# Performance work log

Measured on AMD Instinct MI355X. Metric: run time of the kernel, lower is better.

The kernel has to match this reference:

```python
import jax, jax.numpy as jnp
import numpy as np

N, D, K = 10000, 784, 16          # nodes, input feat dim, num_neighbors
E = N * (K - 1)                   # edges
H = 128                           # hidden width in all MLPs
SIZES = [784, 128, 2]             # node_sizes


def setup_inputs() -> dict:
    key = jax.random.key(0)
    ks = jax.random.split(key, 24)
    w = lambda k, shape: jax.random.normal(k, shape, jnp.float32) * 0.02
    inp = {
        "x": jax.random.normal(ks[0], (N, D), jnp.float32),
        "edge_attr": jax.random.uniform(ks[1], (E, 1), jnp.float32),
        "idxs": jax.random.randint(ks[2], (N, K - 1), 0, N, dtype=jnp.int32),
    }
    # Layer 1: in=784, msg_size=784, out=128
    inp["l1_msg_w1"] = w(ks[3], (D + 1, H));      inp["l1_msg_b1"] = jnp.zeros((H,), jnp.float32)
    inp["l1_msg_w2"] = w(ks[4], (H, D));          inp["l1_msg_b2"] = jnp.zeros((D,), jnp.float32)
    inp["l1_node_w1"] = w(ks[5], (D + D, H));     inp["l1_node_b1"] = jnp.zeros((H,), jnp.float32)
    inp["l1_node_w2"] = w(ks[6], (H, 128));       inp["l1_node_b2"] = jnp.zeros((128,), jnp.float32)
    # Layer 2: in=128, msg_size=128, out=2
    inp["l2_msg_w1"] = w(ks[7], (128 + 1, H));    inp["l2_msg_b1"] = jnp.zeros((H,), jnp.float32)
    inp["l2_msg_w2"] = w(ks[8], (H, 128));        inp["l2_msg_b2"] = jnp.zeros((128,), jnp.float32)
    inp["l2_node_w1"] = w(ks[9], (128 + 128, H)); inp["l2_node_b1"] = jnp.zeros((H,), jnp.float32)
    inp["l2_node_w2"] = w(ks[10], (H, 2));        inp["l2_node_b2"] = jnp.zeros((2,), jnp.float32)
    return inp


def _mlp(x, w1, b1, w2, b2):
    return jax.nn.relu(x @ w1 + b1) @ w2 + b2


def _node_layer(x, src, edge_attr,
                mw1, mb1, mw2, mb2, nw1, nb1, nw2, nb2):
    # message over edges: cat(x[src], edge_attr) -> MLP   [E, msg_size]
    msg = _mlp(jnp.concatenate([x[src], edge_attr], axis=1), mw1, mb1, mw2, mb2)
    # scatter_mean by src index (faithful to the original, which uses index=src)
    sums = jax.ops.segment_sum(msg, src, num_segments=N)
    cnt = jax.ops.segment_sum(jnp.ones((src.shape[0], 1), msg.dtype), src, num_segments=N)
    agg = jnp.where(cnt > 0, sums / jnp.maximum(cnt, 1.0), 0.0)
    # node update: cat(x, agg_msg) -> MLP
    return _mlp(jnp.concatenate([x, agg], axis=1), nw1, nb1, nw2, nb2)


def reference(x, edge_attr, idxs,
              l1_msg_w1, l1_msg_b1, l1_msg_w2, l1_msg_b2,
              l1_node_w1, l1_node_b1, l1_node_w2, l1_node_b2,
              l2_msg_w1, l2_msg_b1, l2_msg_w2, l2_msg_b2,
              l2_node_w1, l2_node_b1, l2_node_w2, l2_node_b2):
    src = idxs.reshape(-1)  # [E]; dst is unused by the original message computation
    h = _node_layer(x, src, edge_attr,
                    l1_msg_w1, l1_msg_b1, l1_msg_w2, l1_msg_b2,
                    l1_node_w1, l1_node_b1, l1_node_w2, l1_node_b2)
    proj = _node_layer(h, src, edge_attr,
                       l2_msg_w1, l2_msg_b1, l2_msg_w2, l2_msg_b2,
                       l2_node_w1, l2_node_b1, l2_node_w2, l2_node_b2)  # [N, 2]
    # vectorized per-neighbor squared distances (replaces the nested python loop)
    neigh = proj[idxs]                                   # [N, K-1, 2]
    d = jnp.sum((proj[:, None, :] - neigh) ** 2, axis=-1)  # [N, K-1]
    return d.reshape(-1, 1)                              # [N*(K-1), 1]
```

## Files before the change

kernel.cpp:

```cpp
#include <hip/hip_runtime.h>

#define N_NODES 10000
#define E_EDGES 150000
#define KNB     15
#define EBLOCKS 587
#define GEMM_BLOCKS 628

__global__ void count_kernel(const int* __restrict__ idxs, int* __restrict__ cnt, int e) {
    int i = blockIdx.x * blockDim.x + threadIdx.x;
    if (i < e) atomicAdd(&cnt[idxs[i]], 1);
}

__device__ __forceinline__
void gemm_tile2(const float* __restrict__ A, int K,
                const float* __restrict__ Blo, const float* __restrict__ Bhi, int ldB,
                float* __restrict__ C, int ldC, int M,
                int rowBlk, int colBlk) {
    __shared__ float As2[16][34];
    __shared__ float Bs2[16][64];
    int tid = threadIdx.x;
    int tn  = tid & 15, tm = tid >> 4;
    int arow = tid >> 3, acB = (tid & 7) << 1;
    int brow = tid >> 4, bcol = (tid & 15) << 2;
    int rowBase = rowBlk * 32, colBase = colBlk * 64;

    bool half = (Bhi != nullptr) && (colBase >= 128);
    const float* B = half ? Bhi : Blo;
    int bj = colBase - (half ? 128 : 0) + bcol;

    float2 av; float4 bv;
    auto loadA = [&](int k0, float2& dst) {
        int gr = rowBase + arow;
        if (gr < M) dst = *(const float2*)(A + (size_t)gr * K + k0 + acB);
        else { dst.x = dst.y = 0.f; }
    };
    auto loadB = [&](int k0, float4& dst) {
        dst = *(const float4*)(B + (size_t)(k0 + brow) * ldB + bj);
    };
    loadA(0, av); loadB(0, bv);

    float acc[2][4] = {};
    for (int k0 = 0; k0 < K; k0 += 16) {
        __syncthreads();
        As2[acB + 0][arow] = av.x; As2[acB + 1][arow] = av.y;
        *(float4*)&Bs2[brow][bcol] = bv;
        __syncthreads();
        if (k0 + 16 < K) { loadA(k0 + 16, av); loadB(k0 + 16, bv); }
#pragma unroll
        for (int k = 0; k < 16; ++k) {
            float4 b = *(const float4*)&Bs2[k][tn << 2];
            float2 a = *(const float2*)&As2[k][tm << 1];
            acc[0][0] = fmaf(a.x, b.x, acc[0][0]); acc[0][1] = fmaf(a.x, b.y, acc[0][1]);
            acc[0][2] = fmaf(a.x, b.z, acc[0][2]); acc[0][3] = fmaf(a.x, b.w, acc[0][3]);
            acc[1][0] = fmaf(a.y, b.x, acc[1][0]); acc[1][1] = fmaf(a.y, b.y, acc[1][1]);
            acc[1][2] = fmaf(a.y, b.z, acc[1][2]); acc[1][3] = fmaf(a.y, b.w, acc[1][3]);
        }
    }
#pragma unroll
    for (int i = 0; i < 2; ++i) {
        int row = rowBase + tm * 2 + i;
        if (row >= M) continue;
#pragma unroll
        for (int j = 0; j < 4; ++j)
            C[(size_t)row * ldC + colBase + (tn << 2) + j] = acc[i][j];
    }
}

__global__ __launch_bounds__(256)
void scanfold_kernel(const float* __restrict__ mw2, const float* __restrict__ mb2,
                     const float* __restrict__ nw1, const float* __restrict__ nb2,
                     const float* __restrict__ nw2,
                     const float* __restrict__ m2w1, const float* __restrict__ m2b1,
                     const float* __restrict__ m2w2, const float* __restrict__ m2b2,
                     const float* __restrict__ n2w1, const float* __restrict__ n2b1,
                     float* __restrict__ M1, float* __restrict__ M2,
                     float* __restrict__ WH,
                     float* __restrict__ v1, float* __restrict__ v2,
                     float* __restrict__ bu2, float* __restrict__ bx2,
                     const int* __restrict__ cnt, int* __restrict__ eoff,
                     float* __restrict__ maskv, int* __restrict__ fillc) {
    int b = blockIdx.x;
    if (b == 0) {
        __shared__ int ssum[256];
        int tid = threadIdx.x;
        const int CH = 40;
        int base = tid * CH;
        int v[CH]; int s = 0;
#pragma unroll
        for (int q = 0; q < CH; ++q) {
            int i = base + q;
            v[q] = (i < N_NODES) ? cnt[i] : 0;
            s += v[q];
        }
        ssum[tid] = s;
        __syncthreads();
        for (int off = 1; off < 256; off <<= 1) {
            int t = (tid >= off) ? ssum[tid - off] : 0;
            __syncthreads();
            ssum[tid] += t;
            __syncthreads();
        }
        int ex = ssum[tid] - s;
#pragma unroll
        for (int q = 0; q < CH; ++q) {
            int i = base + q;
            if (i < N_NODES) {
                eoff[i]  = ex;
                maskv[i] = (v[q] > 0) ? 1.f : 0.f;
                fillc[i] = 0;
                ex += v[q];
            }
        }
        return;
    }
    b -= 1;
    if (b < 8) {
        gemm_tile2(mw2, 784, nw1 + 784 * 128, nullptr, 128, M1, 128, 128, b >> 1, b & 1);
    } else if (b < 16) {
        int t = b - 8;
        gemm_tile2(m2w2, 128, n2w1 + 128 * 128, nullptr, 128, M2, 128, 128, t >> 1, t & 1);
    } else if (b < 32) {
        int t = b - 16;
        gemm_tile2(nw2, 128, m2w1, n2w1, 128, WH, 256, 128, t >> 2, t & 3);
    } else {
        __shared__ float red[256];
        int t  = (b - 32) >> 1;
        int j  = ((b - 32) & 1) * 64 + (threadIdx.x & 63);
        int kq = threadIdx.x >> 6;
        const float* bvec; const float* Bv; const float* add; float* out; int Kv;
        if (t == 0)      { bvec = mb2;  Bv = nw1 + 784 * 128;  add = nullptr; out = v1;  Kv = 784; }
        else if (t == 1) { bvec = m2b2; Bv = n2w1 + 128 * 128; add = nullptr; out = v2;  Kv = 128; }
        else if (t == 2) { bvec = nb2;  Bv = m2w1;             add = m2b1;    out = bu2; Kv = 128; }
        else             { bvec = nb2;  Bv = n2w1;             add = n2b1;    out = bx2; Kv = 128; }
        float acc = 0.f;
        for (int k = kq; k < Kv; k += 4) acc = fmaf(bvec[k], Bv[k * 128 + j], acc);
        red[threadIdx.x] = acc;
        __syncthreads();
        if (threadIdx.x < 64) {
            float tot = red[threadIdx.x] + red[threadIdx.x + 64] +
                        red[threadIdx.x + 128] + red[threadIdx.x + 192];
            out[j] = tot + (add ? add[j] : 0.f);
        }
    }
}

__device__ __forceinline__
void gemm784_tile(const float* __restrict__ A,
                  const float* __restrict__ B0, const float* __restrict__ B1,
                  const float* __restrict__ biasLo, const float* __restrict__ biasHi,
                  const float* __restrict__ vhi, const float* __restrict__ rowmask,
                  float* __restrict__ C, int M, int gb) {
    __shared__ float As[16][68];
    __shared__ float Bs[16][64];
    int rb = gb >> 2, cb = gb & 3;
    int tid = threadIdx.x;
    int tm = tid >> 4, tn = tid & 15;
    int arow = tid >> 2, ac4 = (tid & 3) << 2;
    int brow = tid >> 4, bc4 = (tid & 15) << 2;
    int rowBase = rb * 64, colBase = cb * 64;
    bool hi = colBase >= 128;
    const float* B    = hi ? B1 : B0;
    const float* bias = hi ? biasHi : biasLo;
    int bj = ((cb & 1) << 6) + bc4;

    int gr = rowBase + arow; if (gr > M - 1) gr = M - 1;
    const float* Ap = A + (size_t)gr * 784;

    float4 av, bv;
    av = *(const float4*)(Ap + ac4);
    bv = *(const float4*)(B + (size_t)brow * 128 + bj);

    float acc[4][4] = {};
    for (int k0 = 0; k0 < 784; k0 += 16) {
        __syncthreads();
        As[ac4 + 0][arow] = av.x;
        As[ac4 + 1][arow] = av.y;
        As[ac4 + 2][arow] = av.z;
        As[ac4 + 3][arow] = av.w;
        *(float4*)&Bs[brow][bc4] = bv;
        __syncthreads();
        if (k0 + 16 < 784) {
            av = *(const float4*)(Ap + k0 + 16 + ac4);
            bv = *(const float4*)(B + (size_t)(k0 + 16 + brow) * 128 + bj);
        }
#pragma unroll
        for (int k = 0; k < 16; ++k) {
            float4 a = *(const float4*)&As[k][tm << 2];
            float4 b = *(const float4*)&Bs[k][tn << 2];
            acc[0][0] = fmaf(a.x, b.x, acc[0][0]); acc[0][1] = fmaf(a.x, b.y, acc[0][1]);
            acc[0][2] = fmaf(a.x, b.z, acc[0][2]); acc[0][3] = fmaf(a.x, b.w, acc[0][3]);
            acc[1][0] = fmaf(a.y, b.x, acc[1][0]); acc[1][1] = fmaf(a.y, b.y, acc[1][1]);
            acc[1][2] = fmaf(a.y, b.z, acc[1][2]); acc[1][3] = fmaf(a.y, b.w, acc[1][3]);
            acc[2][0] = fmaf(a.z, b.x, acc[2][0]); acc[2][1] = fmaf(a.z, b.y, acc[2][1]);
            acc[2][2] = fmaf(a.z, b.z, acc[2][2]); acc[2][3] = fmaf(a.z, b.w, acc[2][3]);
            acc[3][0] = fmaf(a.w, b.x, acc[3][0]); acc[3][1] = fmaf(a.w, b.y, acc[3][1]);
            acc[3][2] = fmaf(a.w, b.z, acc[3][2]); acc[3][3] = fmaf(a.w, b.w, acc[3][3]);
        }
    }

#pragma unroll
    for (int i = 0; i < 4; ++i) {
        int row = rowBase + (tm << 2) + i;
        if (row >= M) continue;
        float rm = hi ? rowmask[row] : 0.f;
#pragma unroll
        for (int j = 0; j < 4; ++j) {
            int gcol = colBase + (tn << 2) + j;
            int cj   = gcol & 127;
            float v = acc[i][j] + bias[cj];
            if (hi) v = fmaf(rm, vhi[cj], v);
            C[(size_t)row * 256 + gcol] = v;
        }
    }
}

__global__ __launch_bounds__(256)
void fillgemm_kernel(const int* __restrict__ idxs, const float* __restrict__ ea,
                     const int* __restrict__ eoff, int* __restrict__ fillc,
                     float* __restrict__ eas,
                     const float* __restrict__ A,
                     const float* __restrict__ B0, const float* __restrict__ B1,
                     const float* __restrict__ biasLo, const float* __restrict__ biasHi,
                     const float* __restrict__ vhi, const float* __restrict__ rowmask,
                     float* __restrict__ C, int M) {
    int gb = blockIdx.x;
    if (gb < EBLOCKS) {
        int i = gb * 256 + threadIdx.x;
        if (i < E_EDGES) {
            int s = idxs[i];
            int p = atomicAdd(&fillc[s], 1);
            eas[eoff[s] + p] = ea[i];
        }
        return;
    }
    gemm784_tile(A, B0, B1, biasLo, biasHi, vhi, rowmask, C, M, gb - EBLOCKS);
}

__global__ __launch_bounds__(256)
void tail16_kernel(const float* __restrict__ UX1, const float* __restrict__ w1last,
                   const float* __restrict__ eas, const int* __restrict__ eoff,
                   const int* __restrict__ cnt, const float* __restrict__ maskv,
                   const float* __restrict__ M1, const float* __restrict__ WH,
                   const float* __restrict__ bu2, const float* __restrict__ bx2,
                   const float* __restrict__ v2,
                   const float* __restrict__ w2last, const float* __restrict__ M2,
                   const float* __restrict__ pw, const float* __restrict__ pb,
                   float* __restrict__ UX2, float* __restrict__ proj) {
    __shared__ float Bs[16][264];
    __shared__ float mhT[128][18];
    __shared__ float ts[16][132];
    __shared__ float ebuf[1024];
    int rowBase = blockIdx.x * 16;
    int tid = threadIdx.x;
    int tm2 = tid >> 5;
    int tn  = tid & 31;

    auto msg_phase = [&](const float* __restrict__ U, const float* __restrict__ wl) {
        int d = tid & 127, sub = tid >> 7;
        float w = wl[d];
        float uu[8], sum[8];
        int es[8], ec[8];
#pragma unroll
        for (int it = 0; it < 8; ++it) {
            int n  = rowBase + it * 2 + sub;
            ec[it] = cnt[n];
            es[it] = eoff[n];
            uu[it] = U[(size_t)n * 256 + d];
            sum[it] = 0.f;
        }
        int ebase = eoff[rowBase];
        int eend  = (rowBase + 16 < N_NODES) ? eoff[rowBase + 16] : E_EDGES;
        for (int w0 = ebase; w0 < eend; w0 += 1024) {
            int wlen = min(1024, eend - w0);
            __syncthreads();
            for (int q = tid; q < wlen; q += 256) ebuf[q] = eas[w0 + q];
            __syncthreads();
#pragma unroll
            for (int it = 0; it < 8; ++it) {
                int lo = max(es[it], w0), hiE = min(es[it] + ec[it], w0 + wlen);
                for (int e = lo; e < hiE; ++e)
                    sum[it] += fmaxf(fmaf(ebuf[e - w0], w, uu[it]), 0.f);
            }
        }
#pragma unroll
        for (int it = 0; it < 8; ++it)
            mhT[d][it * 2 + sub] = (ec[it] > 0) ? sum[it] / (float)ec[it] : 0.f;
    };

    msg_phase(UX1, w1last);
    __syncthreads();

    {
        float acc[2][4] = {};
        for (int k0 = 0; k0 < 128; k0 += 16) {
            int kr = tid >> 4, c8 = (tid & 15) << 3;
            *(float4*)&Bs[kr][c8]     = *(const float4*)(M1 + (size_t)(k0 + kr) * 128 + c8);
            *(float4*)&Bs[kr][c8 + 4] = *(const float4*)(M1 + (size_t)(k0 + kr) * 128 + c8 + 4);
            __syncthreads();
#pragma unroll
            for (int k = 0; k < 16; ++k) {
                float2 a = *(const float2*)&mhT[k0 + k][tm2 << 1];
                float4 b = *(const float4*)&Bs[k][tn << 2];
                acc[0][0] = fmaf(a.x, b.x, acc[0][0]); acc[0][1] = fmaf(a.x, b.y, acc[0][1]);
                acc[0][2] = fmaf(a.x, b.z, acc[0][2]); acc[0][3] = fmaf(a.x, b.w, acc[0][3]);
                acc[1][0] = fmaf(a.y, b.x, acc[1][0]); acc[1][1] = fmaf(a.y, b.y, acc[1][1]);
                acc[1][2] = fmaf(a.y, b.z, acc[1][2]); acc[1][3] = fmaf(a.y, b.w, acc[1][3]);
            }
            __syncthreads();
        }
#pragma unroll
        for (int i = 0; i < 2; ++i) {
            int row = rowBase + (tm2 << 1) + i;
            float4 xn = *(const float4*)(UX1 + (size_t)row * 256 + 128 + (tn << 2));
            float4 o;
            o.x = fmaxf(acc[i][0] + xn.x, 0.f);
            o.y = fmaxf(acc[i][1] + xn.y, 0.f);
            o.z = fmaxf(acc[i][2] + xn.z, 0.f);
            o.w = fmaxf(acc[i][3] + xn.w, 0.f);
            *(float4*)&ts[(tm2 << 1) + i][tn << 2] = o;
        }
    }

    {
        float acc[2][8] = {};
        for (int k0 = 0; k0 < 128; k0 += 16) {
            int kr = tid >> 4, c4 = (tid & 15) << 2;
#pragma unroll
            for (int p = 0; p < 4; ++p)
                *(float4*)&Bs[kr][c4 + p * 64] =
                    *(const float4*)(WH + (size_t)(k0 + kr) * 256 + c4 + p * 64);
            __syncthreads();
#pragma unroll
            for (int k = 0; k < 16; ++k) {
                float4 b0 = *(const float4*)&Bs[k][tn << 3];
                float4 b1 = *(const float4*)&Bs[k][(tn << 3) + 4];
                float br[8] = {b0.x, b0.y, b0.z, b0.w, b1.x, b1.y, b1.z, b1.w};
#pragma unroll
                for (int i = 0; i < 2; ++i) {
                    float a = ts[(tm2 << 1) + i][k0 + k];
#pragma unroll
                    for (int j = 0; j < 8; ++j)
                        acc[i][j] = fmaf(a, br[j], acc[i][j]);
                }
            }
            __syncthreads();
        }
        bool hi = tn >= 16;
        const float* bias = hi ? bx2 : bu2;
#pragma unroll
        for (int i = 0; i < 2; ++i) {
            int row = rowBase + (tm2 << 1) + i;
            float rm = maskv[row];
            float4 o0, o1; float* po0 = (float*)&o0; float* po1 = (float*)&o1;
#pragma unroll
            for (int j = 0; j < 4; ++j) {
                int cj0 = ((tn << 3) + j) & 127, cj1 = ((tn << 3) + 4 + j) & 127;
                float q0 = acc[i][j]     + bias[cj0];
                float q1 = acc[i][4 + j] + bias[cj1];
                if (hi) { q0 = fmaf(rm, v2[cj0], q0); q1 = fmaf(rm, v2[cj1], q1); }
                po0[j] = q0; po1[j] = q1;
            }
            float* orow = UX2 + (size_t)row * 256 + (tn << 3);
            *(float4*)orow       = o0;
            *(float4*)(orow + 4) = o1;
        }
    }
    __syncthreads();

    msg_phase(UX2, w2last);

    {
        float acc[2][4] = {};
        for (int k0 = 0; k0 < 128; k0 += 16) {
            int kr = tid >> 4, c8 = (tid & 15) << 3;
            *(float4*)&Bs[kr][c8]     = *(const float4*)(M2 + (size_t)(k0 + kr) * 128 + c8);
            *(float4*)&Bs[kr][c8 + 4] = *(const float4*)(M2 + (size_t)(k0 + kr) * 128 + c8 + 4);
            __syncthreads();
#pragma unroll
            for (int k = 0; k < 16; ++k) {
                float2 a = *(const float2*)&mhT[k0 + k][tm2 << 1];
                float4 b = *(const float4*)&Bs[k][tn << 2];
                acc[0][0] = fmaf(a.x, b.x, acc[0][0]); acc[0][1] = fmaf(a.x, b.y, acc[0][1]);
                acc[0][2] = fmaf(a.x, b.z, acc[0][2]); acc[0][3] = fmaf(a.x, b.w, acc[0][3]);
                acc[1][0] = fmaf(a.y, b.x, acc[1][0]); acc[1][1] = fmaf(a.y, b.y, acc[1][1]);
                acc[1][2] = fmaf(a.y, b.z, acc[1][2]); acc[1][3] = fmaf(a.y, b.w, acc[1][3]);
            }
            __syncthreads();
        }
        float pp0[2], pp1[2];
#pragma unroll
        for (int i = 0; i < 2; ++i) {
            int row = rowBase + (tm2 << 1) + i;
            float4 xn = *(const float4*)(UX2 + (size_t)row * 256 + 128 + (tn << 2));
            float t0 = fmaxf(acc[i][0] + xn.x, 0.f);
            float t1 = fmaxf(acc[i][1] + xn.y, 0.f);
            float t2 = fmaxf(acc[i][2] + xn.z, 0.f);
            float t3 = fmaxf(acc[i][3] + xn.w, 0.f);
            int c = tn << 2;
            pp0[i] = fmaf(t3, pw[2*(c+3)],   fmaf(t2, pw[2*(c+2)],   fmaf(t1, pw[2*(c+1)],   t0 * pw[2*c])));
            pp1[i] = fmaf(t3, pw[2*(c+3)+1], fmaf(t2, pw[2*(c+2)+1], fmaf(t1, pw[2*(c+1)+1], t0 * pw[2*c+1])));
        }
        for (int off = 16; off > 0; off >>= 1) {
            pp0[0] += __shfl_xor(pp0[0], off, 64);
            pp0[1] += __shfl_xor(pp0[1], off, 64);
            pp1[0] += __shfl_xor(pp1[0], off, 64);
            pp1[1] += __shfl_xor(pp1[1], off, 64);
        }
        if (tn == 0) {
#pragma unroll
            for (int i = 0; i < 2; ++i) {
                int row = rowBase + (tm2 << 1) + i;
                proj[2 * row]     = pp0[i] + pb[0];
                proj[2 * row + 1] = pp1[i] + pb[1];
            }
        }
    }
}

__global__ void dist_kernel(const float* __restrict__ proj, const int* __restrict__ idxs,
                            float* __restrict__ out, int e) {
    int i = blockIdx.x * blockDim.x + threadIdx.x;
    if (i >= e) return;
    int n = i / KNB;
    int m = idxs[i];
    float2 pn = *(const float2*)(proj + 2 * n);
    float2 pm = *(const float2*)(proj + 2 * m);
    float dx = pn.x - pm.x;
    float dy = pn.y - pm.y;
    out[i] = dx * dx + dy * dy;
}

extern "C" void kernel_launch(void* const* d_in, const int* in_sizes, int n_in,
                              void* d_out, int out_size, void* d_ws, size_t ws_size,
                              hipStream_t stream) {
    (void)in_sizes; (void)n_in; (void)out_size; (void)ws_size;
    const float* x    = (const float*)d_in[0];
    const float* eatt = (const float*)d_in[1];
    const int*   idxs = (const int*)d_in[2];
    const float* mw1  = (const float*)d_in[3];
    const float* mb1  = (const float*)d_in[4];
    const float* mw2  = (const float*)d_in[5];
    const float* mb2  = (const float*)d_in[6];
    const float* nw1  = (const float*)d_in[7];
    const float* nb1  = (const float*)d_in[8];
    const float* nw2  = (const float*)d_in[9];
    const float* nb2  = (const float*)d_in[10];
    const float* m2w1 = (const float*)d_in[11];
    const float* m2b1 = (const float*)d_in[12];
    const float* m2w2 = (const float*)d_in[13];
    const float* m2b2 = (const float*)d_in[14];
    const float* n2w1 = (const float*)d_in[15];
    const float* n2b1 = (const float*)d_in[16];
    const float* n2w2 = (const float*)d_in[17];
    const float* n2b2 = (const float*)d_in[18];
    float* out = (float*)d_out;

    float* fws   = (float*)d_ws;
    float* UX1   = fws;
    float* UX2   = fws + 2560000;
    float* proj  = fws + 5120000;
    float* maskv = fws + 5140000;
    float* eas   = fws + 5150016;
    float* M1    = fws + 5300016;
    float* M2    = fws + 5316400;
    float* WH    = fws + 5332784;
    float* v1    = fws + 5365552;
    float* v2    = fws + 5365680;
    float* bu2   = fws + 5365808;
    float* bx2   = fws + 5365936;
    int*   cnt   = (int*)(fws + 5366064);
    int*   fillc = cnt + N_NODES;
    int*   eoff  = fillc + N_NODES;

    hipMemsetAsync(cnt, 0, N_NODES * sizeof(int), stream);
    count_kernel<<<EBLOCKS, 256, 0, stream>>>(idxs, cnt, E_EDGES);

    scanfold_kernel<<<41, 256, 0, stream>>>(mw2, mb2, nw1, nb2, nw2,
                                            m2w1, m2b1, m2w2, m2b2, n2w1, n2b1,
                                            M1, M2, WH, v1, v2, bu2, bx2,
                                            cnt, eoff, maskv, fillc);

    fillgemm_kernel<<<EBLOCKS + GEMM_BLOCKS, 256, 0, stream>>>(
        idxs, eatt, eoff, fillc, eas,
        x, mw1, nw1, mb1, nb1, v1, maskv, UX1, N_NODES);

    tail16_kernel<<<625, 256, 0, stream>>>(UX1, mw1 + 784 * 128, eas, eoff, cnt, maskv,
                                           M1, WH, bu2, bx2, v2,
                                           m2w1 + 128 * 128, M2,
                                           n2w2, n2b2,
                                           UX2, proj);

    dist_kernel<<<EBLOCKS, 256, 0, stream>>>(proj, idxs, out, E_EDGES);
}
```

Before: 303.0 us.

## Replace FP32 784-wide GEMM with split-bf16 MFMA using pre-transposed weights

The FP32 SIMT tile GEMM over x (10000x784) times the stacked first-layer weights is replaced with an MFMA bf16 GEMM. Each operand is split into three bf16 parts and six cross products are accumulated to keep close to FP32 accuracy. Extra scanfold blocks transpose and pre-split the weights into a bf16 buffer that reuses the UX2 workspace region. The edge-fill blocks now come after the GEMM blocks. This trades extra split arithmetic and six MFMAs per step for the matrix cores' much higher throughput.

```diff
diff --git a/kernel.cpp b/kernel.cpp
--- a/kernel.cpp
+++ b/kernel.cpp
@@ -4,7 +4,22 @@
 #define E_EDGES 150000
 #define KNB     15
 #define EBLOCKS 587
-#define GEMM_BLOCKS 628
+#define GEMMB   626
+
+typedef unsigned short u16;
+typedef __bf16 bf16x8 __attribute__((ext_vector_type(8)));
+typedef float  f32x4  __attribute__((ext_vector_type(4)));
+
+__device__ __forceinline__ void split3(float a, u16& h, u16& m, u16& l) {
+    unsigned u = __float_as_uint(a);
+    unsigned t = u + 0x7FFFu + ((u >> 16) & 1u);
+    h = (u16)(t >> 16);
+    float r1 = a - __uint_as_float(t & 0xFFFF0000u);
+    unsigned u1 = __float_as_uint(r1);
+    m = (u16)(u1 >> 16);
+    float r2 = r1 - __uint_as_float(u1 & 0xFFFF0000u);
+    l = (u16)(__float_as_uint(r2) >> 16);
+}
 
 __global__ void count_kernel(const int* __restrict__ idxs, int* __restrict__ cnt, int e) {
     int i = blockIdx.x * blockDim.x + threadIdx.x;
@@ -78,8 +93,39 @@
                      float* __restrict__ v1, float* __restrict__ v2,
                      float* __restrict__ bu2, float* __restrict__ bx2,
                      const int* __restrict__ cnt, int* __restrict__ eoff,
-                     float* __restrict__ maskv, int* __restrict__ fillc) {
+                     float* __restrict__ maskv, int* __restrict__ fillc,
+                     const float* __restrict__ mw1, u16* __restrict__ Bt) {
     int b = blockIdx.x;
+    if (b >= 41) {
+        __shared__ float Lt[800][17];
+        int b2 = b - 41;
+        int colBase = b2 * 16;
+        const float* S = (colBase < 128) ? mw1 : nw1;
+        int sc = colBase & 127;
+        int tid = threadIdx.x;
+        for (int i = 0; i < 50; ++i) {
+            int row = (tid >> 4) + i * 16;
+            Lt[row][tid & 15] = (row < 784) ? S[(size_t)row * 128 + sc + (tid & 15)] : 0.f;
+        }
+        __syncthreads();
+        int col = tid >> 4, o = tid & 15;
+        size_t dbase = (size_t)(colBase + col) * 800;
+        for (int o2 = o; o2 < 100; o2 += 16) {
+            u16 hs[8], ms[8], ls[8];
+#pragma unroll
+            for (int e = 0; e < 8; ++e) split3(Lt[o2 * 8 + e][col], hs[e], ms[e], ls[e]);
+            auto pk = [](const u16* s) {
+                uint4 v;
+                v.x = s[0] | ((unsigned)s[1] << 16); v.y = s[2] | ((unsigned)s[3] << 16);
+                v.z = s[4] | ((unsigned)s[5] << 16); v.w = s[6] | ((unsigned)s[7] << 16);
+                return v;
+            };
+            *(uint4*)(Bt +          dbase + o2 * 8) = pk(hs);
+            *(uint4*)(Bt + 204800 + dbase + o2 * 8) = pk(ms);
+            *(uint4*)(Bt + 409600 + dbase + o2 * 8) = pk(ls);
+        }
+        return;
+    }
     if (b == 0) {
         __shared__ int ssum[256];
         int tid = threadIdx.x;
@@ -145,95 +191,129 @@
 }
 
 __device__ __forceinline__
-void gemm784_tile(const float* __restrict__ A,
-                  const float* __restrict__ B0, const float* __restrict__ B1,
-                  const float* __restrict__ biasLo, const float* __restrict__ biasHi,
-                  const float* __restrict__ vhi, const float* __restrict__ rowmask,
-                  float* __restrict__ C, int M, int gb) {
-    __shared__ float As[16][68];
-    __shared__ float Bs[16][64];
-    int rb = gb >> 2, cb = gb & 3;
-    int tid = threadIdx.x;
-    int tm = tid >> 4, tn = tid & 15;
-    int arow = tid >> 2, ac4 = (tid & 3) << 2;
-    int brow = tid >> 4, bc4 = (tid & 15) << 2;
-    int rowBase = rb * 64, colBase = cb * 64;
-    bool hi = colBase >= 128;
-    const float* B    = hi ? B1 : B0;
-    const float* bias = hi ? biasHi : biasLo;
-    int bj = ((cb & 1) << 6) + bc4;
-
-    int gr = rowBase + arow; if (gr > M - 1) gr = M - 1;
-    const float* Ap = A + (size_t)gr * 784;
-
-    float4 av, bv;
-    av = *(const float4*)(Ap + ac4);
-    bv = *(const float4*)(B + (size_t)brow * 128 + bj);
-
-    float acc[4][4] = {};
-    for (int k0 = 0; k0 < 784; k0 += 16) {
-        __syncthreads();
-        As[ac4 + 0][arow] = av.x;
-        As[ac4 + 1][arow] = av.y;
-        As[ac4 + 2][arow] = av.z;
-        As[ac4 + 3][arow] = av.w;
-        *(float4*)&Bs[brow][bc4] = bv;
-        __syncthreads();
-        if (k0 + 16 < 784) {
-            av = *(const float4*)(Ap + k0 + 16 + ac4);
-            bv = *(const float4*)(B + (size_t)(k0 + 16 + brow) * 128 + bj);
-        }
-#pragma unroll
-        for (int k = 0; k < 16; ++k) {
-            float4 a = *(const float4*)&As[k][tm << 2];
-            float4 b = *(const float4*)&Bs[k][tn << 2];
-            acc[0][0] = fmaf(a.x, b.x, acc[0][0]); acc[0][1] = fmaf(a.x, b.y, acc[0][1]);
-            acc[0][2] = fmaf(a.x, b.z, acc[0][2]); acc[0][3] = fmaf(a.x, b.w, acc[0][3]);
-            acc[1][0] = fmaf(a.y, b.x, acc[1][0]); acc[1][1] = fmaf(a.y, b.y, acc[1][1]);
-            acc[1][2] = fmaf(a.y, b.z, acc[1][2]); acc[1][3] = fmaf(a.y, b.w, acc[1][3]);
-            acc[2][0] = fmaf(a.z, b.x, acc[2][0]); acc[2][1] = fmaf(a.z, b.y, acc[2][1]);
-            acc[2][2] = fmaf(a.z, b.z, acc[2][2]); acc[2][3] = fmaf(a.z, b.w, acc[2][3]);
-            acc[3][0] = fmaf(a.w, b.x, acc[3][0]); acc[3][1] = fmaf(a.w, b.y, acc[3][1]);
-            acc[3][2] = fmaf(a.w, b.z, acc[3][2]); acc[3][3] = fmaf(a.w, b.w, acc[3][3]);
-        }
-    }
-
-#pragma unroll
-    for (int i = 0; i < 4; ++i) {
-        int row = rowBase + (tm << 2) + i;
-        if (row >= M) continue;
-        float rm = hi ? rowmask[row] : 0.f;
-#pragma unroll
-        for (int j = 0; j < 4; ++j) {
-            int gcol = colBase + (tn << 2) + j;
-            int cj   = gcol & 127;
-            float v = acc[i][j] + bias[cj];
-            if (hi) v = fmaf(rm, vhi[cj], v);
-            C[(size_t)row * 256 + gcol] = v;
-        }
-    }
+void gemm_mfma(const float* __restrict__ A, const u16* __restrict__ Bt,
+               const float* __restrict__ biasLo, const float* __restrict__ biasHi,
+               const float* __restrict__ vhi, const float* __restrict__ rowmask,
+               float* __restrict__ C, int gb) {
+    __shared__ u16 Bs[3][8][64][8];
+    __shared__ u16 As[3][2][64][8];
+    int tid  = threadIdx.x;
+    int lane = tid & 63, w = tid >> 6;
+    int rb = gb >> 1, cb = gb & 1;
+    int rowBase = rb * 32, colBase = cb * 128;
+
+    int ar  = tid >> 3;
+    int akc = (tid & 7) << 2;
+    int arow = rowBase + ar; if (arow > N_NODES - 1) arow = N_NODES - 1;
+    const float* Ap = A + (size_t)arow * 784;
+    int aL  = (ar & 15) + ((akc >> 3) << 4);
+    int aE  = akc & 4;
+    int aRf = ar >> 4;
+
+    size_t bsrc[6]; int bp[6], bcf[6];
+#pragma unroll
+    for (int j = 0; j < 6; ++j) {
+        int wid = w * 6 + j;
+        int p = wid >> 3, cf = wid & 7;
+        bp[j] = p; bcf[j] = cf;
+        bsrc[j] = (size_t)p * 204800 +
+                  (size_t)(colBase + cf * 16 + (lane & 15)) * 800 + ((lane >> 4) << 3);
+    }
+
+    float4 av; uint4 bv[6];
+    auto loadT = [&](int k0) {
+        int kk = akc + k0; if (kk >= 784) kk = 0;
+        av = *(const float4*)(Ap + kk);
+#pragma unroll
+        for (int j = 0; j < 6; ++j) bv[j] = *(const uint4*)(Bt + bsrc[j] + k0);
+    };
+    ushort4 a3[3];
+    auto splitA = [&]() {
+        u16 h, m, l;
+        split3(av.x, h, m, l); a3[0].x = h; a3[1].x = m; a3[2].x = l;
+        split3(av.y, h, m, l); a3[0].y = h; a3[1].y = m; a3[2].y = l;
+        split3(av.z, h, m, l); a3[0].z = h; a3[1].z = m; a3[2].z = l;
+        split3(av.w, h, m, l); a3[0].w = h; a3[1].w = m; a3[2].w = l;
+    };
+
+    f32x4 acc[2][2];
+    const f32x4 fz = {0.f, 0.f, 0.f, 0.f};
+    acc[0][0] = fz; acc[0][1] = fz; acc[1][0] = fz; acc[1][1] = fz;
+
+    loadT(0); splitA();
+    for (int t = 0; t < 25; ++t) {
+        __syncthreads();
+#pragma unroll
+        for (int p = 0; p < 3; ++p)
+            *(ushort4*)&As[p][aRf][aL][aE] = a3[p];
+#pragma unroll
+        for (int j = 0; j < 6; ++j)
+            *(uint4*)&Bs[bp[j]][bcf[j]][lane][0] = bv[j];
+        __syncthreads();
+        if (t < 24) loadT((t + 1) << 5);
+
+        bf16x8 af[2][3], bfr[2][3];
+#pragma unroll
+        for (int rf = 0; rf < 2; ++rf)
+#pragma unroll
+            for (int p = 0; p < 3; ++p)
+                af[rf][p] = *reinterpret_cast<const bf16x8*>(&As[p][rf][lane][0]);
+#pragma unroll
+        for (int cf = 0; cf < 2; ++cf)
+#pragma unroll
+            for (int q = 0; q < 3; ++q)
+                bfr[cf][q] = *reinterpret_cast<const bf16x8*>(&Bs[q][w * 2 + cf][lane][0]);
+
+#define TERM(p, q) \
+        acc[0][0] = __builtin_amdgcn_mfma_f32_16x16x32_bf16(af[0][p], bfr[0][q], acc[0][0], 0, 0, 0); \
+        acc[0][1] = __builtin_amdgcn_mfma_f32_16x16x32_bf16(af[0][p], bfr[1][q], acc[0][1], 0, 0, 0); \
+        acc[1][0] = __builtin_amdgcn_mfma_f32_16x16x32_bf16(af[1][p], bfr[0][q], acc[1][0], 0, 0, 0); \
+        acc[1][1] = __builtin_amdgcn_mfma_f32_16x16x32_bf16(af[1][p], bfr[1][q], acc[1][1], 0, 0, 0);
+        TERM(0, 0) TERM(0, 1) TERM(1, 0) TERM(0, 2) TERM(1, 1) TERM(2, 0)
+#undef TERM
+        if (t < 24) splitA();
+    }
+
+    const float* bias = cb ? biasHi : biasLo;
+#pragma unroll
+    for (int rf = 0; rf < 2; ++rf)
+#pragma unroll
+        for (int cf = 0; cf < 2; ++cf) {
+            int col = colBase + w * 32 + cf * 16 + (lane & 15);
+            int cj  = col & 127;
+            float bb = bias[cj];
+            float vh = cb ? vhi[cj] : 0.f;
+#pragma unroll
+            for (int r = 0; r < 4; ++r) {
+                int row = rowBase + rf * 16 + ((lane >> 4) << 2) + r;
+                if (row < N_NODES) {
+                    float v = acc[rf][cf][r] + bb;
+                    if (cb) v = fmaf(rowmask[row], vh, v);
+                    C[(size_t)row * 256 + col] = v;
+                }
+            }
+        }
 }
 
 __global__ __launch_bounds__(256)
 void fillgemm_kernel(const int* __restrict__ idxs, const float* __restrict__ ea,
                      const int* __restrict__ eoff, int* __restrict__ fillc,
                      float* __restrict__ eas,
-                     const float* __restrict__ A,
-                     const float* __restrict__ B0, const float* __restrict__ B1,
+                     const float* __restrict__ A, const u16* __restrict__ Bt,
                      const float* __restrict__ biasLo, const float* __restrict__ biasHi,
                      const float* __restrict__ vhi, const float* __restrict__ rowmask,
-                     float* __restrict__ C, int M) {
+                     float* __restrict__ C) {
     int gb = blockIdx.x;
-    if (gb < EBLOCKS) {
-        int i = gb * 256 + threadIdx.x;
-        if (i < E_EDGES) {
-            int s = idxs[i];
-            int p = atomicAdd(&fillc[s], 1);
-            eas[eoff[s] + p] = ea[i];
-        }
+    if (gb < GEMMB) {
+        gemm_mfma(A, Bt, biasLo, biasHi, vhi, rowmask, C, gb);
         return;
     }
-    gemm784_tile(A, B0, B1, biasLo, biasHi, vhi, rowmask, C, M, gb - EBLOCKS);
+    int i = (gb - GEMMB) * 256 + threadIdx.x;
+    if (i < E_EDGES) {
+        int s = idxs[i];
+        int p = atomicAdd(&fillc[s], 1);
+        eas[eoff[s] + p] = ea[i];
+    }
 }
 
 __global__ __launch_bounds__(256)
@@ -471,18 +551,19 @@
     int*   cnt   = (int*)(fws + 5366064);
     int*   fillc = cnt + N_NODES;
     int*   eoff  = fillc + N_NODES;
+    u16*   Bt    = (u16*)(fws + 2560000);
 
     hipMemsetAsync(cnt, 0, N_NODES * sizeof(int), stream);
     count_kernel<<<EBLOCKS, 256, 0, stream>>>(idxs, cnt, E_EDGES);
 
-    scanfold_kernel<<<41, 256, 0, stream>>>(mw2, mb2, nw1, nb2, nw2,
+    scanfold_kernel<<<57, 256, 0, stream>>>(mw2, mb2, nw1, nb2, nw2,
                                             m2w1, m2b1, m2w2, m2b2, n2w1, n2b1,
                                             M1, M2, WH, v1, v2, bu2, bx2,
-                                            cnt, eoff, maskv, fillc);
-
-    fillgemm_kernel<<<EBLOCKS + GEMM_BLOCKS, 256, 0, stream>>>(
+                                            cnt, eoff, maskv, fillc, mw1, Bt);
+
+    fillgemm_kernel<<<GEMMB + EBLOCKS, 256, 0, stream>>>(
         idxs, eatt, eoff, fillc, eas,
-        x, mw1, nw1, mb1, nb1, v1, maskv, UX1, N_NODES);
+        x, Bt, mb1, nb1, v1, maskv, UX1);
 
     tail16_kernel<<<625, 256, 0, stream>>>(UX1, mw1 + 784 * 128, eas, eoff, cnt, maskv,
                                            M1, WH, bu2, bx2, v2,
```

Measured after the change: 382.0 us. 26.1% more time.
